# Performance work log

Hardware: AMD Instinct MI355X
Metric: run time of the kernel (lower is better)

## Reference

```python
import jax, jax.numpy as jnp
import numpy as np

N, E = 50000, 400000
N_INP, H, D = 256, 4, 32
HID = H * D
TN, TE, L, N_OUT = 4, 6, 2, 16
SQRT_D = float(np.sqrt(D))


def setup_inputs() -> dict:
    key = jax.random.key(0)
    ks = jax.random.split(key, 16)
    s = 0.05
    return {
        "x": jax.random.normal(ks[0], (N, N_INP), jnp.float32),
        "adapt_W": jax.random.normal(ks[1], (TN, N_INP, HID), jnp.float32) * s,
        "adapt_b": jnp.zeros((TN, HID), jnp.float32),
        "Wk": jax.random.normal(ks[2], (L, TN, HID, HID), jnp.float32) * s,
        "Wq": jax.random.normal(ks[3], (L, TN, HID, HID), jnp.float32) * s,
        "Wv": jax.random.normal(ks[4], (L, TN, HID, HID), jnp.float32) * s,
        "pri": jnp.ones((L, H, TE), jnp.float32),
        "Wa": jax.random.normal(ks[5], (L, H, TE, D, D), jnp.float32) * s,
        "Wm": jax.random.normal(ks[6], (L, H, TE, D, D), jnp.float32) * s,
        "Wla": jax.random.normal(ks[7], (L, TN, HID, HID), jnp.float32) * s,
        "skip": jnp.ones((L, TN), jnp.float32),
        "gamma": jnp.ones((L, HID), jnp.float32),
        "beta": jnp.zeros((L, HID), jnp.float32),
        "out_W": jax.random.normal(ks[8], (HID, N_OUT), jnp.float32) * s,
        "out_b": jnp.zeros((N_OUT,), jnp.float32),
        "ntype": jax.random.randint(ks[9], (N,), 0, TN),
        "etype": jax.random.randint(ks[10], (E,), 0, TE),
        "src": jax.random.randint(ks[11], (E,), 0, N),
        "dst": jax.random.randint(ks[12], (E,), 0, N),
    }


def typed_linear(x, W, types):
    # out[i] = x[i] @ W[types[i]]  (TypedLinear / per-type nn.Linear loop)
    out = jnp.zeros((x.shape[0], W.shape[-1]), x.dtype)
    for t in range(W.shape[0]):
        out = jnp.where((types == t)[:, None], x @ W[t], out)
    return out


def hgt_layer(h, ntype, etype, src, dst, Wk, Wq, Wv, pri, Wa, Wm, Wla, skip, gamma, beta):
    k = typed_linear(h, Wk, ntype).reshape(N, H, D)
    q = typed_linear(h, Wq, ntype).reshape(N, H, D)
    v = typed_linear(h, Wv, ntype).reshape(N, H, D)
    k_e, q_e, v_e = k[src], q[dst], v[src]  # [E,H,D] gathers
    a = jnp.zeros((E, H), h.dtype)
    m = jnp.zeros((E, H, D), h.dtype)
    for t in range(TE):  # small fixed loop over edge types (relation matrices)
        sel = etype == t
        kw = jnp.einsum('ehd,hdo->eho', k_e, Wa[:, t])
        sc = (kw * q_e).sum(-1) * pri[:, t][None, :] / SQRT_D  # [E,H]
        a = jnp.where(sel[:, None], sc, a)
        mt = jnp.einsum('ehd,hdo->eho', v_e, Wm[:, t])
        m = jnp.where(sel[:, None, None], mt, m)
    # edge softmax over incoming edges of each destination node
    amax = jax.ops.segment_max(a, dst, num_segments=N)
    ex = jnp.exp(a - amax[dst])
    den = jax.ops.segment_sum(ex, dst, num_segments=N)
    attn = ex / den[dst]
    agg = jax.ops.segment_sum(m * attn[:, :, None], dst, num_segments=N).reshape(N, HID)
    ha = typed_linear(agg, Wla, ntype)
    alpha = jax.nn.sigmoid(skip)[ntype][:, None]
    out = ha * alpha + h * (1.0 - alpha)
    mu = out.mean(-1, keepdims=True)
    var = jnp.mean((out - mu) ** 2, -1, keepdims=True)
    return (out - mu) / jnp.sqrt(var + 1e-5) * gamma + beta


def forward(x, adapt_W, adapt_b, Wk, Wq, Wv, pri, Wa, Wm, Wla, skip, gamma, beta, out_W, out_b, ntype, etype, src, dst):
    # per-node-type adapt linear + exact GELU
    h = typed_linear(x, adapt_W, ntype) + adapt_b[ntype]
    h = jax.nn.gelu(h, approximate=False)
    for l in range(L):
        h = hgt_layer(h, ntype, etype, src, dst, Wk[l], Wq[l], Wv[l], pri[l], Wa[l], Wm[l], Wla[l], skip[l], gamma[l], beta[l])
    return h @ out_W + out_b


def reference(x, adapt_W, adapt_b, Wk, Wq, Wv, pri, Wa, Wm, Wla, skip, gamma, beta, out_W, out_b, ntype, etype, src, dst):
    return forward(x, adapt_W, adapt_b, Wk, Wq, Wv, pri, Wa, Wm, Wla, skip, gamma, beta, out_W, out_b, ntype, etype, src, dst)
```

## Files before the change

### kernel.cpp

```cpp
#include <hip/hip_runtime.h>
#include <hip/hip_bf16.h>
#include <math.h>

#define NN   50000
#define EE   400000
#define NINP 256
#define HH   4
#define DD   32
#define HIDD 128
#define TNN  4
#define TEE  6
#define LLL  2
#define NOUTT 16
#define NB   196


typedef __attribute__((ext_vector_type(8))) short bf16x8;
typedef __attribute__((ext_vector_type(4))) float f32x4;

__device__ __forceinline__ float bf_lo(unsigned u) { return __uint_as_float(u << 16); }
__device__ __forceinline__ float bf_hi(unsigned u) { return __uint_as_float(u & 0xFFFF0000u); }
__device__ __forceinline__ unsigned f2bf(float f) {
    unsigned u = __float_as_uint(f);
    u += 0x7FFFu + ((u >> 16) & 1u);
    return (u >> 16);
}

__global__ void k_init(int* __restrict__ deg, int* __restrict__ cur, int* __restrict__ ncnt,
                       int* __restrict__ ncur, int* __restrict__ nperm) {
    int i = blockIdx.x * 256 + threadIdx.x;
    if (i < NN) { deg[i] = 0; cur[i] = 0; }
    if (i < 16) { ncnt[i] = 0; ncur[i] = 0; }
    if (i < NN + 512) nperm[i] = -1;
}

__global__ void k_count_edges(const int* __restrict__ dst, int* __restrict__ deg) {
    int e = blockIdx.x * 256 + threadIdx.x;
    if (e < EE) atomicAdd(&deg[dst[e]], 1);
}
__global__ void k_count_types(const int* __restrict__ ntype, int* __restrict__ ncnt) {
    int n = blockIdx.x * 256 + threadIdx.x;
    int lane = threadIdx.x & 63;
    int t = (n < NN) ? ntype[n] : -1;
#pragma unroll
    for (int tt = 0; tt < TNN; tt++) {
        unsigned long long mask = __ballot(t == tt);
        if (mask && lane == (__ffsll((unsigned long long)mask) - 1))
            atomicAdd(&ncnt[tt], __popcll(mask));
    }
}
__global__ void k_scan1(const int* __restrict__ deg, int* __restrict__ bsum) {
    int i = blockIdx.x * 256 + threadIdx.x;
    int lane = threadIdx.x & 63, wv = threadIdx.x >> 6;
    __shared__ int ws[4];
    int x = (i < NN) ? deg[i] : 0;
#pragma unroll
    for (int off = 1; off < 64; off <<= 1) x += __shfl_xor(x, off);
    if (lane == 0) ws[wv] = x;
    __syncthreads();
    if (threadIdx.x == 0) bsum[blockIdx.x] = ws[0] + ws[1] + ws[2] + ws[3];
}
__global__ void k_scan2(const int* __restrict__ bsum, int* __restrict__ bpre,
                        const int* __restrict__ ncnt, int* __restrict__ meta) {
    __shared__ int ws[4];
    int tid = threadIdx.x, lane = tid & 63, wv = tid >> 6;
    int v = (tid < NB) ? bsum[tid] : 0;
    int x = v;
#pragma unroll
    for (int off = 1; off < 64; off <<= 1) {
        int y = __shfl_up(x, off);
        if (lane >= off) x += y;
    }
    if (lane == 63) ws[wv] = x;
    __syncthreads();
    if (tid == 0) { int a = 0; for (int w = 0; w < 4; w++) { int s = ws[w]; ws[w] = a; a += s; } }
    __syncthreads();
    if (tid < NB) bpre[tid] = x - v + ws[wv];
    if (tid == 0) {
        int acc = 0;
        meta[0] = 0;
        for (int t = 0; t < TNN; t++) { acc += ((ncnt[t] + 63) >> 6) << 6; meta[t + 1] = acc; }
    }
}
__global__ void k_scan3(const int* __restrict__ deg, const int* __restrict__ bpre,
                        int* __restrict__ offs) {
    int b = blockIdx.x;
    int tid = threadIdx.x, lane = tid & 63, wv = tid >> 6;
    int i = b * 256 + tid;
    __shared__ int ws[4];
    int v = (i < NN) ? deg[i] : 0;
    int x = v;
#pragma unroll
    for (int off = 1; off < 64; off <<= 1) {
        int y = __shfl_up(x, off);
        if (lane >= off) x += y;
    }
    if (lane == 63) ws[wv] = x;
    __syncthreads();
    if (tid == 0) { int a = 0; for (int w = 0; w < 4; w++) { int s = ws[w]; ws[w] = a; a += s; } }
    __syncthreads();
    if (i < NN) offs[i + 1] = x + ws[wv] + bpre[b];
    if (b == 0 && tid == 0) offs[0] = 0;
}
__global__ void k_scatter_edges(const int* __restrict__ dst, const int* __restrict__ src,
                                const int* __restrict__ etype, const int* __restrict__ offs,
                                int* __restrict__ cur, unsigned* __restrict__ se) {
    int e = blockIdx.x * 256 + threadIdx.x;
    if (e < EE) {
        int d = dst[e];
        int p = atomicAdd(&cur[d], 1);
        se[offs[d] + p] = ((unsigned)src[e] << 3) | (unsigned)etype[e];
    }
}
__global__ void k_scatter_nodes(const int* __restrict__ ntype, const int* __restrict__ meta,
                                int* __restrict__ ncur, int* __restrict__ nperm) {
    int n = blockIdx.x * 256 + threadIdx.x;
    int lane = threadIdx.x & 63;
    int t = (n < NN) ? ntype[n] : -1;
#pragma unroll
    for (int tt = 0; tt < TNN; tt++) {
        unsigned long long mask = __ballot(t == tt);
        if (t == tt) {
            int rank = __popcll(mask & ((1ull << lane) - 1ull));
            int leader = __ffsll((unsigned long long)mask) - 1;
            int b = 0;
            if (rank == 0) b = atomicAdd(&ncur[tt], __popcll(mask));
            b = __shfl(b, leader);
            nperm[meta[tt] + b + rank] = n;
        }
    }
}

__global__ void k_wt(const float* __restrict__ adapt_W, const float* __restrict__ Wk,
                     const float* __restrict__ Wla, unsigned short* __restrict__ adaptT,
                     unsigned short* __restrict__ Wf, unsigned short* __restrict__ WlaT) {
    __shared__ float Ts[64][68];
    int b = blockIdx.x, tid = threadIdx.x;
    const float* src;
    unsigned short* dst;
    int K, kt, nt;
    if (b < 32) {
        int t = b >> 3, tile = b & 7;
        K = 256; kt = tile >> 1; nt = tile & 1;
        src = adapt_W + (size_t)t * 256 * 128;
        dst = adaptT + (size_t)t * 128 * 256;
    } else if (b < 64) {
        int b2 = b - 32, l = b2 >> 4, r = b2 & 15, t = r >> 2, tile = r & 3;
        K = 128; kt = tile >> 1; nt = tile & 1;
        src = Wk + (size_t)(l * 4 + t) * 16384;
        dst = Wf + (size_t)(l * TNN + t) * 1664 * 128;
    } else {
        int b2 = b - 64, l = b2 >> 4, r = b2 & 15, t = r >> 2, tile = r & 3;
        K = 128; kt = tile >> 1; nt = tile & 1;
        src = Wla + (size_t)(l * 4 + t) * 16384;
        dst = WlaT + (size_t)(l * 4 + t) * 16384;
    }
    int k0 = kt * 64, n0 = nt * 64;
#pragma unroll
    for (int it = 0; it < 4; it++) {
        int idx = tid + it * 256;
        int row = idx >> 4, c4 = (idx & 15) * 4;
        *(float4*)(&Ts[row][c4]) = *(const float4*)(src + (size_t)(k0 + row) * 128 + n0 + c4);
    }
    __syncthreads();
#pragma unroll
    for (int it = 0; it < 2; it++) {
        int idx = tid + it * 256;
        int nn = idx >> 3, sg = (idx & 7) * 8;
        uint4 pk;
        pk.x = f2bf(Ts[sg + 0][nn]) | (f2bf(Ts[sg + 1][nn]) << 16);
        pk.y = f2bf(Ts[sg + 2][nn]) | (f2bf(Ts[sg + 3][nn]) << 16);
        pk.z = f2bf(Ts[sg + 4][nn]) | (f2bf(Ts[sg + 5][nn]) << 16);
        pk.w = f2bf(Ts[sg + 6][nn]) | (f2bf(Ts[sg + 7][nn]) << 16);
        *(uint4*)(dst + (size_t)(n0 + nn) * K + k0 + sg) = pk;
    }
}

__global__ void k_comb(const float* __restrict__ Wq, const float* __restrict__ Wa,
                       const float* __restrict__ Wv, const float* __restrict__ Wm,
                       const float* __restrict__ pri, unsigned short* __restrict__ Wf) {
    __shared__ float Ls[128][36];
    __shared__ float Ss[32][36];
    __shared__ unsigned short Ot[32][136];
    int b = blockIdx.x, tid = threadIdx.x;
    int mode = b / 192;
    int rem = b % 192;
    int l = rem / 96;
    int rem2 = rem % 96;
    int t = rem2 / 24;
    int ht = rem2 % 24;
    int hh = ht / 6, te = ht % 6;
    const float* L = (mode == 0 ? Wq : Wv) + ((size_t)(l * TNN + t)) * 16384;
    const float* S = (mode == 0 ? Wa : Wm) + ((size_t)((l * HH + hh) * TEE + te)) * 1024;
    float ps = (mode == 0) ? pri[(l * HH + hh) * TEE + te] * 0.17677669529663687f : 1.0f;
#pragma unroll
    for (int it = 0; it < 4; it++) {
        int idx = tid + it * 256;
        int kk = idx >> 3, c4 = (idx & 7) * 4;
        *(float4*)(&Ls[kk][c4]) = *(const float4*)(L + (size_t)kk * 128 + hh * 32 + c4);
    }
    {
        int r = tid >> 3, c4 = (tid & 7) * 4;
        *(float4*)(&Ss[r][c4]) = *(const float4*)(S + r * 32 + c4);
    }
    __syncthreads();
    int k = tid >> 1, half = tid & 1;
#pragma unroll
    for (int jj = 0; jj < 16; jj++) {
        int j = half * 16 + jj;
        float s = 0.f;
        if (mode == 0) {
#pragma unroll
            for (int o = 0; o < 32; o++) s += Ls[k][o] * Ss[j][o];
        } else {
#pragma unroll
            for (int d = 0; d < 32; d++) s += Ls[k][d] * Ss[d][j];
        }
        Ot[j][k] = (unsigned short)f2bf(s * ps);
    }
    __syncthreads();
    unsigned short* dst = Wf + ((size_t)(l * TNN + t) * 1664 + (mode == 0 ? 128 : 896)) * 128;
#pragma unroll
    for (int it = 0; it < 2; it++) {
        int idx = tid + it * 256;
        int j = idx >> 4, sg = (idx & 15) * 8;
        uint4 pk = *(const uint4*)(&Ot[j][sg]);
        int jg = (hh * 6 + te) * 32 + j;
        *(uint4*)(dst + (size_t)jg * 128 + sg) = pk;
    }
}

template <int K, int NCB, int EPI, int OMODE, int AF32>
__launch_bounds__(256) __global__
void k_gemm(const void* __restrict__ Av, const unsigned short* __restrict__ WT,
            const float* __restrict__ bias, float* __restrict__ Yf,
            unsigned short* __restrict__ Yb, const int* __restrict__ nperm,
            const int* __restrict__ meta, const float* __restrict__ skipv,
            const float* __restrict__ gamma, const float* __restrict__ beta,
            float* __restrict__ hres, unsigned short* __restrict__ hbout) {
    __shared__ __align__(16) char smem[52224];
    unsigned short* Ab = (unsigned short*)smem;
    unsigned short* Bs = (unsigned short*)(smem + 17408);
    float* Cb = (float*)(smem + 17408);
    const int WIDTH = NCB * 128;
    int row0 = blockIdx.x * 64;
    if (row0 >= meta[4]) return;
    int t = 0;
    while (t < 3 && row0 >= meta[t + 1]) t++;
    const unsigned short* WTt = WT + (size_t)t * WIDTH * K;
    int tid = threadIdx.x;
    int lane = tid & 63, w = tid >> 6;
    int m = lane & 15, q = lane >> 4;

#pragma unroll 1
    for (int cb = 0; cb < NCB; cb++) {
        f32x4 acc[4][2];
#pragma unroll
        for (int rt = 0; rt < 4; rt++)
#pragma unroll
            for (int ct = 0; ct < 2; ct++) acc[rt][ct] = (f32x4){0.f, 0.f, 0.f, 0.f};
#pragma unroll
        for (int kc = 0; kc < K / 128; kc++) {
            __syncthreads();
            if (NCB == 1 || cb == 0) {
                if (AF32) {
                    const float* A = (const float*)Av;
#pragma unroll
                    for (int it = 0; it < 8; it++) {
                        int idx = tid + it * 256;
                        int r = idx >> 5, c4 = (idx & 31) * 4;
                        int node = nperm[row0 + r];
                        float4 v = make_float4(0.f, 0.f, 0.f, 0.f);
                        if (node >= 0)
                            v = *(const float4*)(A + (size_t)node * K + kc * 128 + c4);
                        uint2 pk;
                        pk.x = f2bf(v.x) | (f2bf(v.y) << 16);
                        pk.y = f2bf(v.z) | (f2bf(v.w) << 16);
                        *(uint2*)(Ab + r * 136 + c4) = pk;
                    }
                } else {
                    const unsigned short* A = (const unsigned short*)Av;
#pragma unroll
                    for (int it = 0; it < 4; it++) {
                        int idx = tid + it * 256;
                        int r = idx >> 4, sg = idx & 15;
                        int node = nperm[row0 + r];
                        uint4 v = make_uint4(0, 0, 0, 0);
                        if (node >= 0)
                            v = *(const uint4*)(A + (size_t)node * K + kc * 128 + sg * 8);
                        *(uint4*)(Ab + r * 136 + sg * 8) = v;
                    }
                }
            }
#pragma unroll
            for (int it = 0; it < 8; it++) {
                int idx = tid + it * 256;
                int n = idx >> 4, sg = idx & 15;
                *(uint4*)(Bs + n * 136 + sg * 8) =
                    *(const uint4*)(WTt + (size_t)(cb * 128 + n) * K + kc * 128 + sg * 8);
            }
            __syncthreads();
#pragma unroll
            for (int k0 = 0; k0 < 128; k0 += 32) {
                bf16x8 b0 = *(const bf16x8*)(Bs + (w * 32 + m) * 136 + k0 + q * 8);
                bf16x8 b1 = *(const bf16x8*)(Bs + (w * 32 + 16 + m) * 136 + k0 + q * 8);
#pragma unroll
                for (int rt = 0; rt < 4; rt++) {
                    bf16x8 a = *(const bf16x8*)(Ab + (rt * 16 + m) * 136 + k0 + q * 8);
                    acc[rt][0] = __builtin_amdgcn_mfma_f32_16x16x32_bf16(a, b0, acc[rt][0], 0, 0, 0);
                    acc[rt][1] = __builtin_amdgcn_mfma_f32_16x16x32_bf16(a, b1, acc[rt][1], 0, 0, 0);
                }
            }
        }
        if (EPI == 2) {
            __syncthreads();
#pragma unroll
            for (int rt = 0; rt < 4; rt++)
#pragma unroll
                for (int ct = 0; ct < 2; ct++)
#pragma unroll
                    for (int r = 0; r < 4; r++)
                        Cb[(rt * 16 + q * 4 + r) * 132 + (w * 2 + ct) * 16 + m] = acc[rt][ct][r];
            __syncthreads();
            float alpha = 1.0f / (1.0f + __expf(-skipv[t]));
            int off = lane * 2;
            float2 g2 = *(const float2*)(gamma + off);
            float2 b2 = *(const float2*)(beta + off);
#pragma unroll 1
            for (int it = 0; it < 16; it++) {
                int row = w * 16 + it;
                int node = nperm[row0 + row];
                if (node < 0) continue;
                float ax = Cb[row * 132 + off];
                float ay = Cb[row * 132 + off + 1];
                float2 h2 = *(const float2*)(hres + (size_t)node * 128 + off);
                float ox = ax * alpha + h2.x * (1.f - alpha);
                float oy = ay * alpha + h2.y * (1.f - alpha);
                float s = ox + oy;
#pragma unroll
                for (int mm = 1; mm < 64; mm <<= 1) s += __shfl_xor(s, mm);
                float mu = s * (1.0f / 128.0f);
                float dx = ox - mu, dy = oy - mu;
                float v2 = dx * dx + dy * dy;
#pragma unroll
                for (int mm = 1; mm < 64; mm <<= 1) v2 += __shfl_xor(v2, mm);
                float rs = rsqrtf(v2 * (1.0f / 128.0f) + 1e-5f);
                float vx = dx * rs * g2.x + b2.x;
                float vy = dy * rs * g2.y + b2.y;
                *(float2*)(hres + (size_t)node * 128 + off) = make_float2(vx, vy);
                *(unsigned*)(hbout + (size_t)node * 128 + off) = f2bf(vx) | (f2bf(vy) << 16);
            }
        } else {
#pragma unroll 1
            for (int hf = 0; hf < 2; hf++) {
                __syncthreads();
                if ((w >> 1) == hf) {
#pragma unroll
                    for (int rt = 0; rt < 4; rt++)
#pragma unroll
                        for (int ct = 0; ct < 2; ct++)
#pragma unroll
                            for (int r = 0; r < 4; r++)
                                Cb[(rt * 16 + q * 4 + r) * 68 + (w & 1) * 32 + ct * 16 + m] =
                                    acc[rt][ct][r];
                }
                __syncthreads();
#pragma unroll
                for (int it = 0; it < 4; it++) {
                    int idx = tid + it * 256;
                    int row = idx >> 4, c4 = (idx & 15) * 4;
                    int node = nperm[row0 + row];
                    if (node < 0) continue;
                    float4 v = *(const float4*)(Cb + row * 68 + c4);
                    if (EPI == 1) {
                        float4 bv = *(const float4*)(bias + t * 128 + hf * 64 + c4);
                        v.x += bv.x; v.y += bv.y; v.z += bv.z; v.w += bv.w;
                        const float is2 = 0.70710678118654752f;
                        v.x = 0.5f * v.x * (1.f + erff(v.x * is2));
                        v.y = 0.5f * v.y * (1.f + erff(v.y * is2));
                        v.z = 0.5f * v.z * (1.f + erff(v.z * is2));
                        v.w = 0.5f * v.w * (1.f + erff(v.w * is2));
                    }
                    int col = cb * 128 + hf * 64 + c4;
                    if (OMODE == 0 || OMODE == 2)
                        *(float4*)(Yf + (size_t)node * WIDTH + col) = v;
                    if (OMODE == 1 || OMODE == 2) {
                        uint2 pk;
                        pk.x = f2bf(v.x) | (f2bf(v.y) << 16);
                        pk.y = f2bf(v.z) | (f2bf(v.w) << 16);
                        *(uint2*)(Yb + (size_t)node * WIDTH + col) = pk;
                    }
                }
            }
        }
    }
}

__global__ void k_edge(const unsigned short* __restrict__ kqv,
                       const int* __restrict__ offs, const unsigned* __restrict__ se,
                       unsigned short* __restrict__ aggb) {
    int lane = threadIdx.x & 63;
    int wid = blockIdx.x * (blockDim.x >> 6) + (threadIdx.x >> 6);
    int nw = gridDim.x * (blockDim.x >> 6);
    int h = lane >> 4;
    int i2 = (lane & 15) * 2;
    int hoff = h * 32 + i2;
    for (int n = wid; n < NN; n += nw) {
        int e0 = offs[n], e1 = offs[n + 1];
        float ax = 0.f, ay = 0.f, den = 0.f;
        const unsigned short* qrow = kqv + (size_t)n * 1664 + 128;
        int s[4], t[4];
#pragma unroll
        for (int u = 0; u < 4; u++) {
            s[u] = 0; t[u] = 0;
            if (e0 + u < e1) { unsigned p0 = se[e0 + u]; s[u] = p0 >> 3; t[u] = p0 & 7; }
        }
        int j = e0;
        while (j + 3 < e1) {
            unsigned ku[4], qu[4], vu[4];
#pragma unroll
            for (int u = 0; u < 4; u++) {
                int to = (h * 6 + t[u]) * 32 + i2;
                ku[u] = *(const unsigned*)(kqv + (size_t)s[u] * 1664 + hoff);
                qu[u] = *(const unsigned*)(qrow + to);
                vu[u] = *(const unsigned*)(kqv + (size_t)s[u] * 1664 + 896 + to);
            }
            int jn = j + 4;
#pragma unroll
            for (int u = 0; u < 4; u++)
                if (jn + u < e1) { unsigned p0 = se[jn + u]; s[u] = p0 >> 3; t[u] = p0 & 7; }
            float p[4];
#pragma unroll
            for (int u = 0; u < 4; u++)
                p[u] = bf_lo(ku[u]) * bf_lo(qu[u]) + bf_hi(ku[u]) * bf_hi(qu[u]);
#pragma unroll
            for (int mm = 1; mm < 16; mm <<= 1) {
#pragma unroll
                for (int u = 0; u < 4; u++) p[u] += __shfl_xor(p[u], mm);
            }
#pragma unroll
            for (int u = 0; u < 4; u++) {
                float ex = __expf(p[u]);
                den += ex;
                ax += ex * bf_lo(vu[u]);
                ay += ex * bf_hi(vu[u]);
            }
            j = jn;
        }
        for (int u = 0; j < e1; j++, u++) {
            int to = (h * 6 + t[u]) * 32 + i2;
            unsigned ku = *(const unsigned*)(kqv + (size_t)s[u] * 1664 + hoff);
            unsigned qu = *(const unsigned*)(qrow + to);
            unsigned vu = *(const unsigned*)(kqv + (size_t)s[u] * 1664 + 896 + to);
            float p0 = bf_lo(ku) * bf_lo(qu) + bf_hi(ku) * bf_hi(qu);
            p0 += __shfl_xor(p0, 1);
            p0 += __shfl_xor(p0, 2);
            p0 += __shfl_xor(p0, 4);
            p0 += __shfl_xor(p0, 8);
            float ex = __expf(p0);
            den += ex;
            ax += ex * bf_lo(vu);
            ay += ex * bf_hi(vu);
        }
        float r = (den > 0.f) ? (1.0f / den) : 0.f;
        unsigned pk = f2bf(ax * r) | (f2bf(ay * r) << 16);
        *(unsigned*)(aggb + (size_t)n * 128 + hoff) = pk;
    }
}

__global__ void k_out(const unsigned short* __restrict__ hb, const float* __restrict__ Wo,
                      const float* __restrict__ bo, float* __restrict__ out) {
    __shared__ float Ws[128 * 16];
    int tid = threadIdx.x;
#pragma unroll
    for (int it = 0; it < 2; it++) {
        int idx = (tid + it * 256) * 4;
        *(float4*)(&Ws[idx]) = *(const float4*)(Wo + idx);
    }
    __syncthreads();
    int nl = tid >> 4;
    int o = tid & 15;
    int n = blockIdx.x * 16 + nl;
    float acc = bo[o];
    const unsigned short* hr = hb + (size_t)n * 128;
#pragma unroll
    for (int kk = 0; kk < 128; kk += 8) {
        uint4 hv = *(const uint4*)(hr + kk);
        acc += bf_lo(hv.x) * Ws[(kk + 0) * 16 + o] + bf_hi(hv.x) * Ws[(kk + 1) * 16 + o] +
               bf_lo(hv.y) * Ws[(kk + 2) * 16 + o] + bf_hi(hv.y) * Ws[(kk + 3) * 16 + o] +
               bf_lo(hv.z) * Ws[(kk + 4) * 16 + o] + bf_hi(hv.z) * Ws[(kk + 5) * 16 + o] +
               bf_lo(hv.w) * Ws[(kk + 6) * 16 + o] + bf_hi(hv.w) * Ws[(kk + 7) * 16 + o];
    }
    out[(size_t)n * 16 + o] = acc;
}

extern "C" void kernel_launch(void* const* d_in, const int* in_sizes, int n_in,
                              void* d_out, int out_size, void* d_ws, size_t ws_size,
                              hipStream_t stream) {
    const float* x       = (const float*)d_in[0];
    const float* adapt_W = (const float*)d_in[1];
    const float* adapt_b = (const float*)d_in[2];
    const float* Wk      = (const float*)d_in[3];
    const float* Wq      = (const float*)d_in[4];
    const float* Wv      = (const float*)d_in[5];
    const float* pri     = (const float*)d_in[6];
    const float* Wa      = (const float*)d_in[7];
    const float* Wm      = (const float*)d_in[8];
    const float* Wla     = (const float*)d_in[9];
    const float* skip    = (const float*)d_in[10];
    const float* gamma   = (const float*)d_in[11];
    const float* beta    = (const float*)d_in[12];
    const float* out_W   = (const float*)d_in[13];
    const float* out_b   = (const float*)d_in[14];
    const int* ntype     = (const int*)d_in[15];
    const int* etype     = (const int*)d_in[16];
    const int* src       = (const int*)d_in[17];
    const int* dst       = (const int*)d_in[18];
    float* out = (float*)d_out;

    char* p = (char*)d_ws;
    auto al = [](size_t v) { return (v + 255) & ~(size_t)255; };
    float* h  = (float*)p;          p += al((size_t)NN * 128 * 4);
    unsigned short* hb   = (unsigned short*)p; p += al((size_t)NN * 128 * 2);
    unsigned short* aggb = (unsigned short*)p; p += al((size_t)NN * 128 * 2);
    unsigned short* kqvb = (unsigned short*)p; p += al((size_t)NN * 1664 * 2);
    unsigned short* adaptT = (unsigned short*)p; p += al((size_t)TNN * 128 * 256 * 2);
    unsigned short* WlaT   = (unsigned short*)p; p += al((size_t)LLL * TNN * 16384 * 2);
    unsigned short* Wf     = (unsigned short*)p; p += al((size_t)LLL * TNN * 1664 * 128 * 2);
    int* deg   = (int*)p; p += al((size_t)NN * 4);
    int* offs  = (int*)p; p += al((size_t)(NN + 1) * 4);
    int* cur   = (int*)p; p += al((size_t)NN * 4);
    unsigned* se = (unsigned*)p; p += al((size_t)EE * 4);
    int* nperm = (int*)p; p += al((size_t)(NN + 512) * 4);
    int* bsum  = (int*)p; p += al(256 * 4);
    int* bpre  = (int*)p; p += al(256 * 4);
    int* ncnt  = (int*)p; p += al(64);
    int* ncur  = (int*)p; p += al(64);
    int* meta  = (int*)p; p += al(64);

    k_init<<<(NN + 512 + 255) / 256, 256, 0, stream>>>(deg, cur, ncnt, ncur, nperm);
    k_count_edges<<<(EE + 255) / 256, 256, 0, stream>>>(dst, deg);
    k_count_types<<<(NN + 255) / 256, 256, 0, stream>>>(ntype, ncnt);
    k_scan1<<<NB, 256, 0, stream>>>(deg, bsum);
    k_scan2<<<1, 256, 0, stream>>>(bsum, bpre, ncnt, meta);
    k_scan3<<<NB, 256, 0, stream>>>(deg, bpre, offs);
    k_scatter_edges<<<(EE + 255) / 256, 256, 0, stream>>>(dst, src, etype, offs, cur, se);
    k_scatter_nodes<<<(NN + 255) / 256, 256, 0, stream>>>(ntype, meta, ncur, nperm);

    k_wt<<<96, 256, 0, stream>>>(adapt_W, Wk, Wla, adaptT, Wf, WlaT);
    k_comb<<<384, 256, 0, stream>>>(Wq, Wa, Wv, Wm, pri, Wf);

    const int TILES = NN / 64 + TNN + 1;

    k_gemm<256, 1, 1, 2, 1><<<TILES, 256, 0, stream>>>(
        x, adaptT, adapt_b, h, hb, nperm, meta, nullptr, nullptr, nullptr, nullptr, nullptr);

    for (int l = 0; l < LLL; l++) {
        k_gemm<128, 13, 0, 1, 0><<<TILES, 256, 0, stream>>>(
            hb, Wf + (size_t)l * TNN * 1664 * 128, nullptr, nullptr, kqvb, nperm, meta,
            nullptr, nullptr, nullptr, nullptr, nullptr);

        k_edge<<<4096, 256, 0, stream>>>(kqvb, offs, se, aggb);

        k_gemm<128, 1, 2, 0, 0><<<TILES, 256, 0, stream>>>(
            aggb, WlaT + (size_t)l * TNN * 16384, nullptr, nullptr, nullptr, nperm, meta,
            skip + (size_t)l * TNN, gamma + (size_t)l * HIDD, beta + (size_t)l * HIDD,
            h, hb);
    }

    k_out<<<NN / 16, 256, 0, stream>>>(hb, out_W, out_b, out);
}
```

Baseline: 649.3 us.

## Keep A operand in registers for K=128 GEMMs and write bf16 output via LDS

Adds a k_gemm_reg kernel for the K=128 GEMMs (KQV projection and the Wla/skip/layernorm epilogue). It loads each tile's A fragments directly from global memory into registers once and reuses them across all 13 column blocks, so A no longer goes through shared memory. It also stages the bf16 output in LDS in a single pass instead of two float half-passes, and shrinks shared memory to 34 KB, which may allow more blocks per CU. The cost is 64 extra VGPRs per thread for the A fragments, which could limit occupancy. The original k_gemm is reduced to the f32-input adapt path.

```diff
diff --git a/kernel.cpp b/kernel.cpp
--- a/kernel.cpp
+++ b/kernel.cpp
@@ -235,9 +235,7 @@
 void k_gemm(const void* __restrict__ Av, const unsigned short* __restrict__ WT,
             const float* __restrict__ bias, float* __restrict__ Yf,
             unsigned short* __restrict__ Yb, const int* __restrict__ nperm,
-            const int* __restrict__ meta, const float* __restrict__ skipv,
-            const float* __restrict__ gamma, const float* __restrict__ beta,
-            float* __restrict__ hres, unsigned short* __restrict__ hbout) {
+            const int* __restrict__ meta) {
     __shared__ __align__(16) char smem[52224];
     unsigned short* Ab = (unsigned short*)smem;
     unsigned short* Bs = (unsigned short*)(smem + 17408);
@@ -262,34 +260,20 @@
 #pragma unroll
         for (int kc = 0; kc < K / 128; kc++) {
             __syncthreads();
-            if (NCB == 1 || cb == 0) {
-                if (AF32) {
-                    const float* A = (const float*)Av;
-#pragma unroll
-                    for (int it = 0; it < 8; it++) {
-                        int idx = tid + it * 256;
-                        int r = idx >> 5, c4 = (idx & 31) * 4;
-                        int node = nperm[row0 + r];
-                        float4 v = make_float4(0.f, 0.f, 0.f, 0.f);
-                        if (node >= 0)
-                            v = *(const float4*)(A + (size_t)node * K + kc * 128 + c4);
-                        uint2 pk;
-                        pk.x = f2bf(v.x) | (f2bf(v.y) << 16);
-                        pk.y = f2bf(v.z) | (f2bf(v.w) << 16);
-                        *(uint2*)(Ab + r * 136 + c4) = pk;
-                    }
-                } else {
-                    const unsigned short* A = (const unsigned short*)Av;
-#pragma unroll
-                    for (int it = 0; it < 4; it++) {
-                        int idx = tid + it * 256;
-                        int r = idx >> 4, sg = idx & 15;
-                        int node = nperm[row0 + r];
-                        uint4 v = make_uint4(0, 0, 0, 0);
-                        if (node >= 0)
-                            v = *(const uint4*)(A + (size_t)node * K + kc * 128 + sg * 8);
-                        *(uint4*)(Ab + r * 136 + sg * 8) = v;
-                    }
+            if (AF32) {
+                const float* A = (const float*)Av;
+#pragma unroll
+                for (int it = 0; it < 8; it++) {
+                    int idx = tid + it * 256;
+                    int r = idx >> 5, c4 = (idx & 31) * 4;
+                    int node = nperm[row0 + r];
+                    float4 v = make_float4(0.f, 0.f, 0.f, 0.f);
+                    if (node >= 0)
+                        v = *(const float4*)(A + (size_t)node * K + kc * 128 + c4);
+                    uint2 pk;
+                    pk.x = f2bf(v.x) | (f2bf(v.y) << 16);
+                    pk.y = f2bf(v.z) | (f2bf(v.w) << 16);
+                    *(uint2*)(Ab + r * 136 + c4) = pk;
                 }
             }
 #pragma unroll
@@ -312,15 +296,119 @@
                 }
             }
         }
+#pragma unroll 1
+        for (int hf = 0; hf < 2; hf++) {
+            __syncthreads();
+            if ((w >> 1) == hf) {
+#pragma unroll
+                for (int rt = 0; rt < 4; rt++)
+#pragma unroll
+                    for (int ct = 0; ct < 2; ct++)
+#pragma unroll
+                        for (int r = 0; r < 4; r++)
+                            Cb[(rt * 16 + q * 4 + r) * 68 + (w & 1) * 32 + ct * 16 + m] =
+                                acc[rt][ct][r];
+            }
+            __syncthreads();
+#pragma unroll
+            for (int it = 0; it < 4; it++) {
+                int idx = tid + it * 256;
+                int row = idx >> 4, c4 = (idx & 15) * 4;
+                int node = nperm[row0 + row];
+                if (node < 0) continue;
+                float4 v = *(const float4*)(Cb + row * 68 + c4);
+                if (EPI == 1) {
+                    float4 bv = *(const float4*)(bias + t * 128 + hf * 64 + c4);
+                    v.x += bv.x; v.y += bv.y; v.z += bv.z; v.w += bv.w;
+                    const float is2 = 0.70710678118654752f;
+                    v.x = 0.5f * v.x * (1.f + erff(v.x * is2));
+                    v.y = 0.5f * v.y * (1.f + erff(v.y * is2));
+                    v.z = 0.5f * v.z * (1.f + erff(v.z * is2));
+                    v.w = 0.5f * v.w * (1.f + erff(v.w * is2));
+                }
+                int col = cb * 128 + hf * 64 + c4;
+                if (OMODE == 0 || OMODE == 2)
+                    *(float4*)(Yf + (size_t)node * WIDTH + col) = v;
+                if (OMODE == 1 || OMODE == 2) {
+                    uint2 pk;
+                    pk.x = f2bf(v.x) | (f2bf(v.y) << 16);
+                    pk.y = f2bf(v.z) | (f2bf(v.w) << 16);
+                    *(uint2*)(Yb + (size_t)node * WIDTH + col) = pk;
+                }
+            }
+        }
+    }
+}
+
+template <int NCB, int EPI>
+__launch_bounds__(256) __global__
+void k_gemm_reg(const unsigned short* __restrict__ A, const unsigned short* __restrict__ WT,
+                unsigned short* __restrict__ Yb, const int* __restrict__ nperm,
+                const int* __restrict__ meta, const float* __restrict__ skipv,
+                const float* __restrict__ gamma, const float* __restrict__ beta,
+                float* __restrict__ hres, unsigned short* __restrict__ hbout) {
+    __shared__ __align__(16) char smem[34816];
+    unsigned short* Bs = (unsigned short*)smem;
+    unsigned short* Cb16 = (unsigned short*)smem;
+    float* Cbf = (float*)smem;
+    const int WIDTH = NCB * 128;
+    int row0 = blockIdx.x * 64;
+    if (row0 >= meta[4]) return;
+    int t = 0;
+    while (t < 3 && row0 >= meta[t + 1]) t++;
+    const unsigned short* WTt = WT + (size_t)t * WIDTH * 128;
+    int tid = threadIdx.x;
+    int lane = tid & 63, w = tid >> 6;
+    int m = lane & 15, q = lane >> 4;
+
+    bf16x8 a[4][4];
+#pragma unroll
+    for (int rt = 0; rt < 4; rt++) {
+        int nd = nperm[row0 + rt * 16 + m];
+#pragma unroll
+        for (int kk = 0; kk < 4; kk++) {
+            if (nd >= 0)
+                a[rt][kk] = *(const bf16x8*)(A + (size_t)nd * 128 + kk * 32 + q * 8);
+            else
+                a[rt][kk] = (bf16x8){0, 0, 0, 0, 0, 0, 0, 0};
+        }
+    }
+
+#pragma unroll 1
+    for (int cb = 0; cb < NCB; cb++) {
+        f32x4 acc[4][2];
+#pragma unroll
+        for (int rt = 0; rt < 4; rt++)
+#pragma unroll
+            for (int ct = 0; ct < 2; ct++) acc[rt][ct] = (f32x4){0.f, 0.f, 0.f, 0.f};
+        __syncthreads();
+#pragma unroll
+        for (int it = 0; it < 8; it++) {
+            int idx = tid + it * 256;
+            int n = idx >> 4, sg = idx & 15;
+            *(uint4*)(Bs + n * 136 + sg * 8) =
+                *(const uint4*)(WTt + (size_t)(cb * 128 + n) * 128 + sg * 8);
+        }
+        __syncthreads();
+#pragma unroll
+        for (int kk = 0; kk < 4; kk++) {
+            bf16x8 b0 = *(const bf16x8*)(Bs + (w * 32 + m) * 136 + kk * 32 + q * 8);
+            bf16x8 b1 = *(const bf16x8*)(Bs + (w * 32 + 16 + m) * 136 + kk * 32 + q * 8);
+#pragma unroll
+            for (int rt = 0; rt < 4; rt++) {
+                acc[rt][0] = __builtin_amdgcn_mfma_f32_16x16x32_bf16(a[rt][kk], b0, acc[rt][0], 0, 0, 0);
+                acc[rt][1] = __builtin_amdgcn_mfma_f32_16x16x32_bf16(a[rt][kk], b1, acc[rt][1], 0, 0, 0);
+            }
+        }
+        __syncthreads();
         if (EPI == 2) {
-            __syncthreads();
 #pragma unroll
             for (int rt = 0; rt < 4; rt++)
 #pragma unroll
                 for (int ct = 0; ct < 2; ct++)
 #pragma unroll
                     for (int r = 0; r < 4; r++)
-                        Cb[(rt * 16 + q * 4 + r) * 132 + (w * 2 + ct) * 16 + m] = acc[rt][ct][r];
+                        Cbf[(rt * 16 + q * 4 + r) * 132 + w * 32 + ct * 16 + m] = acc[rt][ct][r];
             __syncthreads();
             float alpha = 1.0f / (1.0f + __expf(-skipv[t]));
             int off = lane * 2;
@@ -331,8 +419,8 @@
                 int row = w * 16 + it;
                 int node = nperm[row0 + row];
                 if (node < 0) continue;
-                float ax = Cb[row * 132 + off];
-                float ay = Cb[row * 132 + off + 1];
+                float ax = Cbf[row * 132 + off];
+                float ay = Cbf[row * 132 + off + 1];
                 float2 h2 = *(const float2*)(hres + (size_t)node * 128 + off);
                 float ox = ax * alpha + h2.x * (1.f - alpha);
                 float oy = ay * alpha + h2.y * (1.f - alpha);
@@ -351,46 +439,23 @@
                 *(unsigned*)(hbout + (size_t)node * 128 + off) = f2bf(vx) | (f2bf(vy) << 16);
             }
         } else {
-#pragma unroll 1
-            for (int hf = 0; hf < 2; hf++) {
-                __syncthreads();
-                if ((w >> 1) == hf) {
-#pragma unroll
-                    for (int rt = 0; rt < 4; rt++)
-#pragma unroll
-                        for (int ct = 0; ct < 2; ct++)
-#pragma unroll
-                            for (int r = 0; r < 4; r++)
-                                Cb[(rt * 16 + q * 4 + r) * 68 + (w & 1) * 32 + ct * 16 + m] =
-                                    acc[rt][ct][r];
-                }
-                __syncthreads();
-#pragma unroll
-                for (int it = 0; it < 4; it++) {
-                    int idx = tid + it * 256;
-                    int row = idx >> 4, c4 = (idx & 15) * 4;
-                    int node = nperm[row0 + row];
-                    if (node < 0) continue;
-                    float4 v = *(const float4*)(Cb + row * 68 + c4);
-                    if (EPI == 1) {
-                        float4 bv = *(const float4*)(bias + t * 128 + hf * 64 + c4);
-                        v.x += bv.x; v.y += bv.y; v.z += bv.z; v.w += bv.w;
-                        const float is2 = 0.70710678118654752f;
-                        v.x = 0.5f * v.x * (1.f + erff(v.x * is2));
-                        v.y = 0.5f * v.y * (1.f + erff(v.y * is2));
-                        v.z = 0.5f * v.z * (1.f + erff(v.z * is2));
-                        v.w = 0.5f * v.w * (1.f + erff(v.w * is2));
-                    }
-                    int col = cb * 128 + hf * 64 + c4;
-                    if (OMODE == 0 || OMODE == 2)
-                        *(float4*)(Yf + (size_t)node * WIDTH + col) = v;
-                    if (OMODE == 1 || OMODE == 2) {
-                        uint2 pk;
-                        pk.x = f2bf(v.x) | (f2bf(v.y) << 16);
-                        pk.y = f2bf(v.z) | (f2bf(v.w) << 16);
-                        *(uint2*)(Yb + (size_t)node * WIDTH + col) = pk;
-                    }
-                }
+#pragma unroll
+            for (int rt = 0; rt < 4; rt++)
+#pragma unroll
+                for (int ct = 0; ct < 2; ct++)
+#pragma unroll
+                    for (int r = 0; r < 4; r++)
+                        Cb16[(rt * 16 + q * 4 + r) * 136 + w * 32 + ct * 16 + m] =
+                            (unsigned short)f2bf(acc[rt][ct][r]);
+            __syncthreads();
+#pragma unroll
+            for (int it = 0; it < 4; it++) {
+                int idx = tid + it * 256;
+                int row = idx >> 4, sg = idx & 15;
+                int node = nperm[row0 + row];
+                if (node < 0) continue;
+                *(uint4*)(Yb + (size_t)node * WIDTH + cb * 128 + sg * 8) =
+                    *(const uint4*)(Cb16 + row * 136 + sg * 8);
             }
         }
     }
@@ -553,17 +618,17 @@
     const int TILES = NN / 64 + TNN + 1;
 
     k_gemm<256, 1, 1, 2, 1><<<TILES, 256, 0, stream>>>(
-        x, adaptT, adapt_b, h, hb, nperm, meta, nullptr, nullptr, nullptr, nullptr, nullptr);
+        x, adaptT, adapt_b, h, hb, nperm, meta);
 
     for (int l = 0; l < LLL; l++) {
-        k_gemm<128, 13, 0, 1, 0><<<TILES, 256, 0, stream>>>(
-            hb, Wf + (size_t)l * TNN * 1664 * 128, nullptr, nullptr, kqvb, nperm, meta,
+        k_gemm_reg<13, 0><<<TILES, 256, 0, stream>>>(
+            hb, Wf + (size_t)l * TNN * 1664 * 128, kqvb, nperm, meta,
             nullptr, nullptr, nullptr, nullptr, nullptr);
 
         k_edge<<<4096, 256, 0, stream>>>(kqvb, offs, se, aggb);
 
-        k_gemm<128, 1, 2, 0, 0><<<TILES, 256, 0, stream>>>(
-            aggb, WlaT + (size_t)l * TNN * 16384, nullptr, nullptr, nullptr, nperm, meta,
+        k_gemm_reg<1, 2><<<TILES, 256, 0, stream>>>(
+            aggb, WlaT + (size_t)l * TNN * 16384, nullptr, nperm, meta,
             skip + (size_t)l * TNN, gamma + (size_t)l * HIDD, beta + (size_t)l * HIDD,
             h, hb);
     }
```

Measured after the change: 609.0 us. 1.07x faster.
